# Kernel optimization log

Hardware: AMD Instinct MI355X
Metric: run time of the kernel (lower is better)

The kernel has to match this reference:

```python
import jax, jax.numpy as jnp
import numpy as np

N_NODES = 50000
N_EDGES = 800000
D = 64  # node_in = edge_out = node_out

def _mlp(h, w1, b1, w2, b2):
    h = jax.nn.relu(h @ w1 + b1)
    return h @ w2 + b2

def setup_inputs() -> dict:
    key = jax.random.key(0)
    ks = jax.random.split(key, 12)
    def lin(k, fan_in, fan_out):
        bound = 1.0 / np.sqrt(fan_in)
        kw, kb = jax.random.split(k)
        w = jax.random.uniform(kw, (fan_in, fan_out), jnp.float32, -bound, bound)
        b = jax.random.uniform(kb, (fan_out,), jnp.float32, -bound, bound)
        return w, b
    x = jax.random.normal(ks[0], (N_NODES, D), jnp.float32)
    edge_index = jax.random.randint(ks[1], (2, N_EDGES), 0, N_NODES, jnp.int64 if jax.config.jax_enable_x64 else jnp.int32)
    edge_attr = jax.random.normal(ks[2], (N_EDGES, D), jnp.float32)
    u = jax.random.normal(ks[3], (1, D), jnp.float32)
    batch = jnp.zeros((N_NODES,), dtype=edge_index.dtype)
    w1a, b1a = lin(ks[4], 2 * D, D)
    w1b, b1b = lin(ks[5], D, D)
    w2a, b2a = lin(ks[6], 2 * D, D)
    w2b, b2b = lin(ks[7], D, D)
    return dict(x=x, edge_index=edge_index, edge_attr=edge_attr, u=u, batch=batch,
                w1a=w1a, b1a=b1a, w1b=w1b, b1b=b1b,
                w2a=w2a, b2a=b2a, w2b=w2b, b2b=b2b)

def reference(x, edge_index, edge_attr, u, batch,
              w1a, b1a, w1b, b1b, w2a, b2a, w2b, b2b):
    row, col = edge_index[0], edge_index[1]
    n = x.shape[0]
    # gather source nodes, concat with edge features: [E, node_in+edge_out]
    h = jnp.concatenate([x[row], edge_attr], axis=1)
    h = _mlp(h, w1a, b1a, w1b, b1b)
    # scatter_mean over destination nodes (zeros for nodes with no incoming edges)
    summed = jax.ops.segment_sum(h, col, num_segments=n)  # [N, D]
    counts = jax.ops.segment_sum(jnp.ones((h.shape[0],), h.dtype), col, num_segments=n)
    agg = summed / jnp.maximum(counts, 1.0)[:, None]
    out = jnp.concatenate([x, agg], axis=1)
    return _mlp(out, w2a, b2a, w2b, b2b)
```

## Files before the change

kernel.cpp:

```cpp
#include <hip/hip_runtime.h>

#define DF 64

typedef __attribute__((ext_vector_type(8))) short bf16x8;
typedef __attribute__((ext_vector_type(2))) short v2s;
typedef __attribute__((ext_vector_type(4))) float f32x4;

__device__ __forceinline__ short f2bf(float f) {
    union { float f; unsigned u; } v; v.f = f;
    unsigned u = v.u;
    u += 0x7FFFu + ((u >> 16) & 1u);
    return (short)(u >> 16);
}

__device__ __forceinline__ float bf2f(unsigned s) {
    union { unsigned u; float f; } v; v.u = s << 16;
    return v.f;
}

__device__ __forceinline__ bf16x8 cvt8(float4 a, float4 b) {
    bf16x8 r;
    r[0] = f2bf(a.x); r[1] = f2bf(a.y); r[2] = f2bf(a.z); r[3] = f2bf(a.w);
    r[4] = f2bf(b.x); r[5] = f2bf(b.y); r[6] = f2bf(b.z); r[7] = f2bf(b.w);
    return r;
}

__device__ __forceinline__ void wave_lds_sync() {
    asm volatile("s_waitcnt lgkmcnt(0)" ::: "memory");
    __builtin_amdgcn_sched_barrier(0);
}

__device__ __forceinline__ void pk_add(short* addr, int val) {
#if __has_builtin(__builtin_amdgcn_global_atomic_fadd_v2bf16)
    __builtin_amdgcn_global_atomic_fadd_v2bf16(
        (__attribute__((address_space(1))) v2s*)addr, *(v2s*)&val);
#else
    unsigned* a = (unsigned*)addr;
    unsigned old = *a, assumed;
    do {
        assumed = old;
        float lo = bf2f(assumed & 0xffffu) + bf2f((unsigned)val & 0xffffu);
        float hi = bf2f(assumed >> 16)     + bf2f((unsigned)val >> 16);
        unsigned nv = (unsigned)(unsigned short)f2bf(lo) |
                      ((unsigned)(unsigned short)f2bf(hi) << 16);
        old = atomicCAS(a, assumed, nv);
    } while (old != assumed);
#endif
}

__global__ __launch_bounds__(256) void prep_weights(
    const float* __restrict__ w1a, const float* __restrict__ w1b,
    const float* __restrict__ w2a, const float* __restrict__ w2b,
    short* __restrict__ w1aT, short* __restrict__ w1bT,
    short* __restrict__ w2aT, short* __restrict__ w2bT)
{
    int gid = blockIdx.x * 256 + threadIdx.x;
    if (gid < 8192) {
        int k = gid >> 6, n = gid & 63;
        w1aT[n * 128 + k] = f2bf(w1a[gid]);
    } else if (gid < 12288) {
        int g = gid - 8192; int k = g >> 6, n = g & 63;
        w1bT[n * 64 + k] = f2bf(w1b[g]);
    } else if (gid < 20480) {
        int g = gid - 12288; int k = g >> 6, n = g & 63;
        w2aT[n * 128 + k] = f2bf(w2a[g]);
    } else if (gid < 24576) {
        int g = gid - 20480; int k = g >> 6, n = g & 63;
        w2bT[n * 64 + k] = f2bf(w2b[g]);
    }
}

__global__ __launch_bounds__(256, 8) void edge_mlp_scatter(
    const float* __restrict__ x, const int* __restrict__ ei,
    const float* __restrict__ ea,
    const short* __restrict__ w1aT, const float* __restrict__ b1a,
    const short* __restrict__ w1bT, const float* __restrict__ b1b,
    short* __restrict__ summedh, float* __restrict__ counts, int E)
{
    __shared__ alignas(16) short lsH[4 * 16 * 72];

    const int t = threadIdx.x;
    const int lane = t & 63;
    const int w = t >> 6;
    const int q = lane >> 4;
    const int m = lane & 15;
    const long base = ((long)blockIdx.x * 4 + w) * 16;

    const long e = base + m;
    const long ec = e < E ? e : (long)(E - 1);
    const int row = ei[ec];

    if (q == 0 && e < E)
        unsafeAtomicAdd(&counts[ei[E + e]], 1.0f);

    const float4* xr = (const float4*)(x + (long)row * DF);
    const float4* er = (const float4*)(ea + ec * DF);
    bf16x8 afr[4];
    afr[0] = cvt8(xr[q * 2],     xr[q * 2 + 1]);
    afr[1] = cvt8(xr[8 + q * 2], xr[8 + q * 2 + 1]);
    afr[2] = cvt8(er[q * 2],     er[q * 2 + 1]);
    afr[3] = cvt8(er[8 + q * 2], er[8 + q * 2 + 1]);

    f32x4 acc[4];
#pragma unroll
    for (int nt = 0; nt < 4; ++nt) {
        float b = b1a[nt * 16 + m];
        f32x4 v = {b, b, b, b};
        acc[nt] = v;
#pragma unroll
        for (int ks = 0; ks < 4; ++ks) {
            bf16x8 bfr = *(const bf16x8*)&w1aT[(nt * 16 + m) * 128 + ks * 32 + q * 8];
            acc[nt] = __builtin_amdgcn_mfma_f32_16x16x32_bf16(afr[ks], bfr, acc[nt], 0, 0, 0);
        }
    }

    short* hw = lsH + w * (16 * 72);
#pragma unroll
    for (int nt = 0; nt < 4; ++nt)
#pragma unroll
        for (int r = 0; r < 4; ++r) {
            float v = acc[nt][r] > 0.f ? acc[nt][r] : 0.f;
            hw[(q * 4 + r) * 72 + nt * 16 + m] = f2bf(v);
        }
    wave_lds_sync();

    bf16x8 a2[2];
    a2[0] = *(const bf16x8*)&hw[m * 72 + q * 8];
    a2[1] = *(const bf16x8*)&hw[m * 72 + 32 + q * 8];

    f32x4 acc2[4];
#pragma unroll
    for (int nt = 0; nt < 4; ++nt) {
        float b = b1b[nt * 16 + m];
        f32x4 v = {b, b, b, b};
        acc2[nt] = v;
#pragma unroll
        for (int ks = 0; ks < 2; ++ks) {
            bf16x8 bfr = *(const bf16x8*)&w1bT[(nt * 16 + m) * 64 + ks * 32 + q * 8];
            acc2[nt] = __builtin_amdgcn_mfma_f32_16x16x32_bf16(a2[ks], bfr, acc2[nt], 0, 0, 0);
        }
    }
    wave_lds_sync();

#pragma unroll
    for (int nt = 0; nt < 4; ++nt)
#pragma unroll
        for (int r = 0; r < 4; ++r)
            hw[(q * 4 + r) * 72 + nt * 16 + m] = f2bf(acc2[nt][r]);
    wave_lds_sync();

    const int p = lane & 31;
    const int* hwi = (const int*)hw;
#pragma unroll
    for (int i = 0; i < 8; ++i) {
        int r2 = (lane >> 5) + 2 * i;
        long eg = base + r2;
        if (eg < E) {
            int dst = ei[E + eg];
            int val = hwi[r2 * 36 + p];
            pk_add(&summedh[(long)dst * DF + 2 * p], val);
        }
    }
}

__global__ __launch_bounds__(256, 8) void node_mlp(
    const float* __restrict__ x, const short* __restrict__ summedh,
    const float* __restrict__ counts,
    const short* __restrict__ w2aT, const float* __restrict__ b2a,
    const short* __restrict__ w2bT, const float* __restrict__ b2b,
    float* __restrict__ out, int NN)
{
    __shared__ alignas(16) short lsH[4 * 16 * 72];

    const int t = threadIdx.x;
    const int lane = t & 63;
    const int w = t >> 6;
    const int q = lane >> 4;
    const int m = lane & 15;
    const long base = ((long)blockIdx.x * 4 + w) * 16;

    const long node = base + m;
    const long nc = node < NN ? node : (long)(NN - 1);

    const float4* xr = (const float4*)(x + nc * DF);
    float c = counts[nc];
    c = c > 1.f ? c : 1.f;
    const float inv = 1.f / c;

    bf16x8 s0 = *(const bf16x8*)&summedh[nc * DF + q * 8];
    bf16x8 s1 = *(const bf16x8*)&summedh[nc * DF + 32 + q * 8];

    bf16x8 afr[4];
    afr[0] = cvt8(xr[q * 2],     xr[q * 2 + 1]);
    afr[1] = cvt8(xr[8 + q * 2], xr[8 + q * 2 + 1]);
#pragma unroll
    for (int i = 0; i < 8; ++i) {
        afr[2][i] = f2bf(bf2f((unsigned short)s0[i]) * inv);
        afr[3][i] = f2bf(bf2f((unsigned short)s1[i]) * inv);
    }

    f32x4 acc[4];
#pragma unroll
    for (int nt = 0; nt < 4; ++nt) {
        float b = b2a[nt * 16 + m];
        f32x4 v = {b, b, b, b};
        acc[nt] = v;
#pragma unroll
        for (int ks = 0; ks < 4; ++ks) {
            bf16x8 bfr = *(const bf16x8*)&w2aT[(nt * 16 + m) * 128 + ks * 32 + q * 8];
            acc[nt] = __builtin_amdgcn_mfma_f32_16x16x32_bf16(afr[ks], bfr, acc[nt], 0, 0, 0);
        }
    }

    short* hw = lsH + w * (16 * 72);
#pragma unroll
    for (int nt = 0; nt < 4; ++nt)
#pragma unroll
        for (int r = 0; r < 4; ++r) {
            float v = acc[nt][r] > 0.f ? acc[nt][r] : 0.f;
            hw[(q * 4 + r) * 72 + nt * 16 + m] = f2bf(v);
        }
    wave_lds_sync();

    bf16x8 a2[2];
    a2[0] = *(const bf16x8*)&hw[m * 72 + q * 8];
    a2[1] = *(const bf16x8*)&hw[m * 72 + 32 + q * 8];

    f32x4 acc2[4];
#pragma unroll
    for (int nt = 0; nt < 4; ++nt) {
        float b = b2b[nt * 16 + m];
        f32x4 v = {b, b, b, b};
        acc2[nt] = v;
#pragma unroll
        for (int ks = 0; ks < 2; ++ks) {
            bf16x8 bfr = *(const bf16x8*)&w2bT[(nt * 16 + m) * 64 + ks * 32 + q * 8];
            acc2[nt] = __builtin_amdgcn_mfma_f32_16x16x32_bf16(a2[ks], bfr, acc2[nt], 0, 0, 0);
        }
    }

#pragma unroll
    for (int r = 0; r < 4; ++r) {
        long n2 = base + q * 4 + r;
        if (n2 < NN) {
#pragma unroll
            for (int nt = 0; nt < 4; ++nt)
                out[n2 * DF + nt * 16 + m] = acc2[nt][r];
        }
    }
}

extern "C" void kernel_launch(void* const* d_in, const int* in_sizes, int n_in,
                              void* d_out, int out_size, void* d_ws, size_t ws_size,
                              hipStream_t stream) {
    const float* x   = (const float*)d_in[0];
    const int*   ei  = (const int*)d_in[1];
    const float* ea  = (const float*)d_in[2];
    const float* w1a = (const float*)d_in[5];
    const float* b1a = (const float*)d_in[6];
    const float* w1b = (const float*)d_in[7];
    const float* b1b = (const float*)d_in[8];
    const float* w2a = (const float*)d_in[9];
    const float* b2a = (const float*)d_in[10];
    const float* w2b = (const float*)d_in[11];
    const float* b2b = (const float*)d_in[12];

    const int NN = in_sizes[0] / DF;
    const int E  = in_sizes[2] / DF;

    char* wsb = (char*)d_ws;
    float* counts  = (float*)wsb;
    short* w1aT    = (short*)(wsb + 262144);
    short* w1bT    = (short*)(wsb + 278528);
    short* w2aT    = (short*)(wsb + 286720);
    short* w2bT    = (short*)(wsb + 303104);
    short* summedh = (short*)(wsb + 311296);

    hipMemsetAsync(counts, 0, (size_t)NN * sizeof(float), stream);
    hipMemsetAsync(summedh, 0, (size_t)NN * DF * sizeof(short), stream);
    prep_weights<<<96, 256, 0, stream>>>(w1a, w1b, w2a, w2b, w1aT, w1bT, w2aT, w2bT);

    int etiles = (E + 15) / 16;
    int eblocks = (etiles + 3) / 4;
    edge_mlp_scatter<<<eblocks, 256, 0, stream>>>(x, ei, ea, w1aT, b1a, w1bT, b1b,
                                                  summedh, counts, E);
    int ntiles = (NN + 15) / 16;
    int nblocks = (ntiles + 3) / 4;
    node_mlp<<<nblocks, 256, 0, stream>>>(x, summedh, counts, w2aT, b2a, w2bT, b2b,
                                          (float*)d_out, NN);
}
```

Baseline: 469.5 us.

## Replace atomic bf16 scatter with counting-sort bucketing and gather-side mean

Adds a histogram and single-block scan that build per-destination CSR offsets. The edge kernel now writes each edge's bf16 MLP output to a sorted slot claimed through an atomic cursor, instead of issuing packed bf16 atomic adds into a per-node sum. The node kernel then sums each node's contiguous rows itself and divides by the count, which also gives fp32 accumulation. This trades the contended atomics for an extra E×64 bf16 buffer, two extra launches, and a serial-ish single-block scan; the old path is kept as a fallback when workspace is too small.

```diff
diff --git a/kernel.cpp b/kernel.cpp
--- a/kernel.cpp
+++ b/kernel.cpp
@@ -70,12 +70,49 @@
     }
 }
 
-__global__ __launch_bounds__(256, 8) void edge_mlp_scatter(
+
+__global__ __launch_bounds__(256) void histogram_k(
+    const int* __restrict__ ei, int* __restrict__ icounts, int E)
+{
+    int gid = blockIdx.x * 256 + threadIdx.x;
+    if (gid < E) atomicAdd(&icounts[ei[E + gid]], 1);
+}
+
+__global__ __launch_bounds__(1024) void scan_offsets(
+    const int* __restrict__ icounts, int* __restrict__ offsets,
+    int* __restrict__ cursor, int NN, int E)
+{
+    __shared__ int part[1024];
+    const int t = threadIdx.x;
+    const int chunk = (NN + 1023) / 1024;
+    const int s = t * chunk;
+    const int e = (s + chunk < NN) ? s + chunk : NN;
+    int sum = 0;
+    for (int i = s; i < e; ++i) sum += icounts[i];
+    part[t] = sum;
+    __syncthreads();
+    for (int off = 1; off < 1024; off <<= 1) {
+        int v = part[t];
+        int o = (t >= off) ? part[t - off] : 0;
+        __syncthreads();
+        part[t] = v + o;
+        __syncthreads();
+    }
+    int run = part[t] - sum;
+    for (int i = s; i < e; ++i) {
+        offsets[i] = run;
+        cursor[i]  = run;
+        run += icounts[i];
+    }
+    if (t == 0) offsets[NN] = E;
+}
+
+__global__ __launch_bounds__(256, 8) void edge_mlp_sorted(
     const float* __restrict__ x, const int* __restrict__ ei,
     const float* __restrict__ ea,
     const short* __restrict__ w1aT, const float* __restrict__ b1a,
     const short* __restrict__ w1bT, const float* __restrict__ b1b,
-    short* __restrict__ summedh, float* __restrict__ counts, int E)
+    short* __restrict__ h_sorted, int* __restrict__ cursor, int E)
 {
     __shared__ alignas(16) short lsH[4 * 16 * 72];
 
@@ -89,9 +126,6 @@
     const long e = base + m;
     const long ec = e < E ? e : (long)(E - 1);
     const int row = ei[ec];
-
-    if (q == 0 && e < E)
-        unsafeAtomicAdd(&counts[ei[E + e]], 1.0f);
 
     const float4* xr = (const float4*)(x + (long)row * DF);
     const float4* er = (const float4*)(ea + ec * DF);
@@ -149,6 +183,207 @@
             hw[(q * 4 + r) * 72 + nt * 16 + m] = f2bf(acc2[nt][r]);
     wave_lds_sync();
 
+    int pos = 0;
+    if (lane < 16) {
+        long eg = base + lane;
+        if (eg < E) pos = atomicAdd(&cursor[ei[E + eg]], 1);
+    }
+    const int* hwi = (const int*)hw;
+    int* hs = (int*)h_sorted;
+#pragma unroll
+    for (int i = 0; i < 2; ++i) {
+        int r = (lane >> 3) + 8 * i;
+        long eg = base + r;
+        int posr = __shfl(pos, r);
+        if (eg < E) {
+            int4 v = *(const int4*)&hwi[r * 36 + (lane & 7) * 4];
+            *(int4*)&hs[(long)posr * 32 + (lane & 7) * 4] = v;
+        }
+    }
+}
+
+__global__ __launch_bounds__(256, 4) void node_mlp_sorted(
+    const float* __restrict__ x, const short* __restrict__ h_sorted,
+    const int* __restrict__ offsets,
+    const short* __restrict__ w2aT, const float* __restrict__ b2a,
+    const short* __restrict__ w2bT, const float* __restrict__ b2b,
+    float* __restrict__ out, int NN)
+{
+    __shared__ alignas(16) short lsH[4 * 16 * 72];
+
+    const int t = threadIdx.x;
+    const int lane = t & 63;
+    const int w = t >> 6;
+    const int q = lane >> 4;
+    const int m = lane & 15;
+    const long base = ((long)blockIdx.x * 4 + w) * 16;
+
+    const long node = base + m;
+    const long nc = node < NN ? node : (long)(NN - 1);
+
+    const int s0 = offsets[nc];
+    const int e0 = offsets[nc + 1];
+    const int cnt = e0 - s0;
+    const float inv = 1.f / (float)(cnt > 1 ? cnt : 1);
+
+    float fs0[8], fs1[8];
+#pragma unroll
+    for (int i = 0; i < 8; ++i) { fs0[i] = 0.f; fs1[i] = 0.f; }
+
+    for (int j = 0; __any(j < cnt); ++j) {
+        if (j < cnt) {
+            const short* rp = &h_sorted[(long)(s0 + j) * DF];
+            bf16x8 r0 = *(const bf16x8*)&rp[q * 8];
+            bf16x8 r1 = *(const bf16x8*)&rp[32 + q * 8];
+#pragma unroll
+            for (int i = 0; i < 8; ++i) {
+                fs0[i] += bf2f((unsigned short)r0[i]);
+                fs1[i] += bf2f((unsigned short)r1[i]);
+            }
+        }
+    }
+
+    const float4* xr = (const float4*)(x + nc * DF);
+    bf16x8 afr[4];
+    afr[0] = cvt8(xr[q * 2],     xr[q * 2 + 1]);
+    afr[1] = cvt8(xr[8 + q * 2], xr[8 + q * 2 + 1]);
+#pragma unroll
+    for (int i = 0; i < 8; ++i) {
+        afr[2][i] = f2bf(fs0[i] * inv);
+        afr[3][i] = f2bf(fs1[i] * inv);
+    }
+
+    f32x4 acc[4];
+#pragma unroll
+    for (int nt = 0; nt < 4; ++nt) {
+        float b = b2a[nt * 16 + m];
+        f32x4 v = {b, b, b, b};
+        acc[nt] = v;
+#pragma unroll
+        for (int ks = 0; ks < 4; ++ks) {
+            bf16x8 bfr = *(const bf16x8*)&w2aT[(nt * 16 + m) * 128 + ks * 32 + q * 8];
+            acc[nt] = __builtin_amdgcn_mfma_f32_16x16x32_bf16(afr[ks], bfr, acc[nt], 0, 0, 0);
+        }
+    }
+
+    short* hw = lsH + w * (16 * 72);
+#pragma unroll
+    for (int nt = 0; nt < 4; ++nt)
+#pragma unroll
+        for (int r = 0; r < 4; ++r) {
+            float v = acc[nt][r] > 0.f ? acc[nt][r] : 0.f;
+            hw[(q * 4 + r) * 72 + nt * 16 + m] = f2bf(v);
+        }
+    wave_lds_sync();
+
+    bf16x8 a2[2];
+    a2[0] = *(const bf16x8*)&hw[m * 72 + q * 8];
+    a2[1] = *(const bf16x8*)&hw[m * 72 + 32 + q * 8];
+
+    f32x4 acc2[4];
+#pragma unroll
+    for (int nt = 0; nt < 4; ++nt) {
+        float b = b2b[nt * 16 + m];
+        f32x4 v = {b, b, b, b};
+        acc2[nt] = v;
+#pragma unroll
+        for (int ks = 0; ks < 2; ++ks) {
+            bf16x8 bfr = *(const bf16x8*)&w2bT[(nt * 16 + m) * 64 + ks * 32 + q * 8];
+            acc2[nt] = __builtin_amdgcn_mfma_f32_16x16x32_bf16(a2[ks], bfr, acc2[nt], 0, 0, 0);
+        }
+    }
+
+#pragma unroll
+    for (int r = 0; r < 4; ++r) {
+        long n2 = base + q * 4 + r;
+        if (n2 < NN) {
+#pragma unroll
+            for (int nt = 0; nt < 4; ++nt)
+                out[n2 * DF + nt * 16 + m] = acc2[nt][r];
+        }
+    }
+}
+
+
+__global__ __launch_bounds__(256, 8) void edge_mlp_scatter(
+    const float* __restrict__ x, const int* __restrict__ ei,
+    const float* __restrict__ ea,
+    const short* __restrict__ w1aT, const float* __restrict__ b1a,
+    const short* __restrict__ w1bT, const float* __restrict__ b1b,
+    short* __restrict__ summedh, float* __restrict__ counts, int E)
+{
+    __shared__ alignas(16) short lsH[4 * 16 * 72];
+
+    const int t = threadIdx.x;
+    const int lane = t & 63;
+    const int w = t >> 6;
+    const int q = lane >> 4;
+    const int m = lane & 15;
+    const long base = ((long)blockIdx.x * 4 + w) * 16;
+
+    const long e = base + m;
+    const long ec = e < E ? e : (long)(E - 1);
+    const int row = ei[ec];
+
+    if (q == 0 && e < E)
+        unsafeAtomicAdd(&counts[ei[E + e]], 1.0f);
+
+    const float4* xr = (const float4*)(x + (long)row * DF);
+    const float4* er = (const float4*)(ea + ec * DF);
+    bf16x8 afr[4];
+    afr[0] = cvt8(xr[q * 2],     xr[q * 2 + 1]);
+    afr[1] = cvt8(xr[8 + q * 2], xr[8 + q * 2 + 1]);
+    afr[2] = cvt8(er[q * 2],     er[q * 2 + 1]);
+    afr[3] = cvt8(er[8 + q * 2], er[8 + q * 2 + 1]);
+
+    f32x4 acc[4];
+#pragma unroll
+    for (int nt = 0; nt < 4; ++nt) {
+        float b = b1a[nt * 16 + m];
+        f32x4 v = {b, b, b, b};
+        acc[nt] = v;
+#pragma unroll
+        for (int ks = 0; ks < 4; ++ks) {
+            bf16x8 bfr = *(const bf16x8*)&w1aT[(nt * 16 + m) * 128 + ks * 32 + q * 8];
+            acc[nt] = __builtin_amdgcn_mfma_f32_16x16x32_bf16(afr[ks], bfr, acc[nt], 0, 0, 0);
+        }
+    }
+
+    short* hw = lsH + w * (16 * 72);
+#pragma unroll
+    for (int nt = 0; nt < 4; ++nt)
+#pragma unroll
+        for (int r = 0; r < 4; ++r) {
+            float v = acc[nt][r] > 0.f ? acc[nt][r] : 0.f;
+            hw[(q * 4 + r) * 72 + nt * 16 + m] = f2bf(v);
+        }
+    wave_lds_sync();
+
+    bf16x8 a2[2];
+    a2[0] = *(const bf16x8*)&hw[m * 72 + q * 8];
+    a2[1] = *(const bf16x8*)&hw[m * 72 + 32 + q * 8];
+
+    f32x4 acc2[4];
+#pragma unroll
+    for (int nt = 0; nt < 4; ++nt) {
+        float b = b1b[nt * 16 + m];
+        f32x4 v = {b, b, b, b};
+        acc2[nt] = v;
+#pragma unroll
+        for (int ks = 0; ks < 2; ++ks) {
+            bf16x8 bfr = *(const bf16x8*)&w1bT[(nt * 16 + m) * 64 + ks * 32 + q * 8];
+            acc2[nt] = __builtin_amdgcn_mfma_f32_16x16x32_bf16(a2[ks], bfr, acc2[nt], 0, 0, 0);
+        }
+    }
+    wave_lds_sync();
+
+#pragma unroll
+    for (int nt = 0; nt < 4; ++nt)
+#pragma unroll
+        for (int r = 0; r < 4; ++r)
+            hw[(q * 4 + r) * 72 + nt * 16 + m] = f2bf(acc2[nt][r]);
+    wave_lds_sync();
+
     const int p = lane & 31;
     const int* hwi = (const int*)hw;
 #pragma unroll
@@ -249,6 +484,7 @@
         }
     }
 }
+
 
 extern "C" void kernel_launch(void* const* d_in, const int* in_sizes, int n_in,
                               void* d_out, int out_size, void* d_ws, size_t ws_size,
@@ -269,23 +505,46 @@
     const int E  = in_sizes[2] / DF;
 
     char* wsb = (char*)d_ws;
-    float* counts  = (float*)wsb;
-    short* w1aT    = (short*)(wsb + 262144);
-    short* w1bT    = (short*)(wsb + 278528);
-    short* w2aT    = (short*)(wsb + 286720);
-    short* w2bT    = (short*)(wsb + 303104);
-    short* summedh = (short*)(wsb + 311296);
-
-    hipMemsetAsync(counts, 0, (size_t)NN * sizeof(float), stream);
-    hipMemsetAsync(summedh, 0, (size_t)NN * DF * sizeof(short), stream);
-    prep_weights<<<96, 256, 0, stream>>>(w1a, w1b, w2a, w2b, w1aT, w1bT, w2aT, w2bT);
+    const size_t need_sorted = 1048576 + (size_t)E * DF * sizeof(short);
 
     int etiles = (E + 15) / 16;
     int eblocks = (etiles + 3) / 4;
-    edge_mlp_scatter<<<eblocks, 256, 0, stream>>>(x, ei, ea, w1aT, b1a, w1bT, b1b,
-                                                  summedh, counts, E);
     int ntiles = (NN + 15) / 16;
     int nblocks = (ntiles + 3) / 4;
-    node_mlp<<<nblocks, 256, 0, stream>>>(x, summedh, counts, w2aT, b2a, w2bT, b2b,
-                                          (float*)d_out, NN);
-}
+
+    if (ws_size >= need_sorted) {
+        int*   icounts = (int*)wsb;
+        int*   offsets = (int*)(wsb + 262144);
+        int*   cursor  = (int*)(wsb + 524288);
+        short* w1aT    = (short*)(wsb + 786432);
+        short* w1bT    = (short*)(wsb + 802816);
+        short* w2aT    = (short*)(wsb + 811008);
+        short* w2bT    = (short*)(wsb + 827392);
+        short* h_sorted= (short*)(wsb + 1048576);
+
+        hipMemsetAsync(icounts, 0, (size_t)NN * sizeof(int), stream);
+        prep_weights<<<96, 256, 0, stream>>>(w1a, w1b, w2a, w2b, w1aT, w1bT, w2aT, w2bT);
+        histogram_k<<<(E + 255) / 256, 256, 0, stream>>>(ei, icounts, E);
+        scan_offsets<<<1, 1024, 0, stream>>>(icounts, offsets, cursor, NN, E);
+        edge_mlp_sorted<<<eblocks, 256, 0, stream>>>(x, ei, ea, w1aT, b1a, w1bT, b1b,
+                                                     h_sorted, cursor, E);
+        node_mlp_sorted<<<nblocks, 256, 0, stream>>>(x, h_sorted, offsets,
+                                                     w2aT, b2a, w2bT, b2b,
+                                                     (float*)d_out, NN);
+    } else {
+        float* counts  = (float*)wsb;
+        short* w1aT    = (short*)(wsb + 262144);
+        short* w1bT    = (short*)(wsb + 278528);
+        short* w2aT    = (short*)(wsb + 286720);
+        short* w2bT    = (short*)(wsb + 303104);
+        short* summedh = (short*)(wsb + 311296);
+
+        hipMemsetAsync(counts, 0, (size_t)NN * sizeof(float), stream);
+        hipMemsetAsync(summedh, 0, (size_t)NN * DF * sizeof(short), stream);
+        prep_weights<<<96, 256, 0, stream>>>(w1a, w1b, w2a, w2b, w1aT, w1bT, w2aT, w2bT);
+        edge_mlp_scatter<<<eblocks, 256, 0, stream>>>(x, ei, ea, w1aT, b1a, w1bT, b1b,
+                                                      summedh, counts, E);
+        node_mlp<<<nblocks, 256, 0, stream>>>(x, summedh, counts, w2aT, b2a, w2bT, b2b,
+                                              (float*)d_out, NN);
+    }
+}
```

Result: slower. 636.3 us (+35.5%).
